# Performance work log

Measured on AMD Instinct MI355X. Metric: run time of the kernel, lower is better.

The kernel has to match this reference:

```python
import jax, jax.numpy as jnp
import numpy as np

B, IN, H = 4096, 1024, 1024

def setup_inputs() -> dict:
    key = jax.random.key(0)
    ks = jax.random.split(key, 8)
    s = 1.0 / np.sqrt(IN + H)  # ~torch Linear init scale
    return {
        "x": jax.random.normal(ks[0], (B, IN), jnp.float32),
        "h_prev": jax.random.normal(ks[1], (B, H), jnp.float32),
        "c_prev": jax.random.normal(ks[2], (B, H), jnp.float32),
        "Wf": jax.random.normal(ks[3], (IN + H, H), jnp.float32) * s,
        "bf": jnp.zeros((H,), jnp.float32),
        "Wi": jax.random.normal(ks[4], (IN + H, H), jnp.float32) * s,
        "bi": jnp.zeros((H,), jnp.float32),
        "Wg": jax.random.normal(ks[5], (IN + H, H), jnp.float32) * s,
        "bg": jnp.zeros((H,), jnp.float32),
        "Wo": jax.random.normal(ks[6], (IN + H, H), jnp.float32) * s,
        "bo": jnp.zeros((H,), jnp.float32),
    }

def reference(x, h_prev, c_prev, Wf, bf, Wi, bi, Wg, bg, Wo, bo):
    combined = jnp.concatenate([x, h_prev], axis=1)          # [B, IN+H]
    # fuse the 4 gate projections into one GEMM: [B, IN+H] x [IN+H, 4H]
    W = jnp.concatenate([Wf, Wi, Wg, Wo], axis=1)            # [IN+H, 4H]
    b = jnp.concatenate([bf, bi, bg, bo], axis=0)            # [4H]
    gates = combined @ W + b                                  # [B, 4H]
    f_t, i_t, g_t, o_t = jnp.split(gates, 4, axis=1)
    f_t = jax.nn.sigmoid(f_t)
    i_t = jax.nn.sigmoid(i_t)
    g_t = jnp.tanh(g_t)
    o_t = jax.nn.sigmoid(o_t)
    c_next = f_t * c_prev + i_t * g_t
    h_next = o_t * jnp.tanh(c_next)
    return (h_next, c_next)
```

## Files before the change

kernel.cpp:

```cpp
#include <hip/hip_runtime.h>

#define B_DIM 4096
#define H_DIM 1024
#define K_DIM 2048
#define NTILE (K_DIM / 64)

typedef unsigned short u16;
typedef unsigned int u32;
typedef __attribute__((ext_vector_type(8))) short short8;
typedef __attribute__((ext_vector_type(4))) float f32x4;

typedef const __attribute__((address_space(1))) void* gas_ptr;
typedef __attribute__((address_space(3))) void* las_ptr;

#define WT_ELEMS (4 * H_DIM * K_DIM)
#define AC_ELEMS (B_DIM * K_DIM)
#define WS_NEEDED ((size_t)(WT_ELEMS + AC_ELEMS) * 2)

__device__ __forceinline__ void gl_lds16(const u16* g, u16* l) {
    __builtin_amdgcn_global_load_lds((gas_ptr)g, (las_ptr)l, 16, 0, 0);
}
__device__ __forceinline__ float bf2f(u16 v) {
    return __builtin_bit_cast(float, (u32)((u32)v << 16));
}
__device__ __forceinline__ u16 f2bf(float f) {
    u32 u = __builtin_bit_cast(u32, f);
    return (u16)((u + 0x7fffu + ((u >> 16) & 1u)) >> 16);
}
__device__ __forceinline__ float sigm(float x) { return 1.0f / (1.0f + __expf(-x)); }
__device__ __forceinline__ float tanh_f(float x) { return 1.0f - 2.0f / (__expf(2.0f * x) + 1.0f); }

__global__ __launch_bounds__(256) void prep_all(const float* __restrict__ x, const float* __restrict__ h,
                                                const float* __restrict__ Wf, const float* __restrict__ Wi,
                                                const float* __restrict__ Wg, const float* __restrict__ Wo,
                                                u16* __restrict__ A, u16* __restrict__ Wt) {
    const int t = threadIdx.x;
    if (blockIdx.x < 4096) {
        int e = (blockIdx.x * 256 + t) * 8;
        int m = e >> 11, c = e & 2047;
        const float* src = (c < 1024) ? (x + (size_t)m * 1024 + c) : (h + (size_t)m * 1024 + (c - 1024));
        float4 v0 = ((const float4*)src)[0], v1 = ((const float4*)src)[1];
        short8 q;
        q[0] = (short)f2bf(v0.x); q[1] = (short)f2bf(v0.y); q[2] = (short)f2bf(v0.z); q[3] = (short)f2bf(v0.w);
        q[4] = (short)f2bf(v1.x); q[5] = (short)f2bf(v1.y); q[6] = (short)f2bf(v1.z); q[7] = (short)f2bf(v1.w);
        *(short8*)(A + e) = q;
    } else {
        const int id = (blockIdx.x - 4096) * 4 + (t >> 6);
        const int l = t & 63;
        const int k0 = (id & 31) * 64, n0 = ((id >> 5) & 15) * 64, g = id >> 9;
        const float* W = (g == 0) ? Wf : (g == 1) ? Wi : (g == 2) ? Wg : Wo;
        const int no = (l & 7) * 8;
        const int ko = (l >> 3) * 8;
        float f[8][8];
#pragma unroll
        for (int j = 0; j < 8; ++j) {
            const float4* s = (const float4*)(W + (size_t)(k0 + ko + j) * H_DIM + n0 + no);
            float4 a = s[0], b = s[1];
            f[j][0] = a.x; f[j][1] = a.y; f[j][2] = a.z; f[j][3] = a.w;
            f[j][4] = b.x; f[j][5] = b.y; f[j][6] = b.z; f[j][7] = b.w;
        }
        u16* dst0 = Wt + (size_t)g * ((size_t)H_DIM * K_DIM) + (size_t)(n0 + no) * K_DIM + k0 + ko;
#pragma unroll
        for (int w2 = 0; w2 < 8; ++w2) {
            short8 q;
#pragma unroll
            for (int j = 0; j < 8; ++j) q[j] = (short)f2bf(f[j][w2]);
            *(short8*)(dst0 + (size_t)w2 * K_DIM) = q;
        }
    }
}

#define PH_OPEN                                                  \
    __builtin_amdgcn_s_barrier();                                \
    asm volatile("s_waitcnt lgkmcnt(0)" ::: "memory");           \
    __builtin_amdgcn_sched_barrier(0);                           \
    __builtin_amdgcn_s_setprio(1)

#define PH_CLOSE                                                 \
    __builtin_amdgcn_s_setprio(0);                               \
    __builtin_amdgcn_sched_barrier(0);                           \
    __builtin_amdgcn_s_barrier();                                \
    __builtin_amdgcn_sched_barrier(0)

#define PH_CLOSE_VM2                                             \
    __builtin_amdgcn_s_setprio(0);                               \
    __builtin_amdgcn_sched_barrier(0);                           \
    asm volatile("s_waitcnt vmcnt(2)" ::: "memory");             \
    __builtin_amdgcn_s_barrier();                                \
    __builtin_amdgcn_sched_barrier(0)

#define PH_CLOSE_VM0                                             \
    __builtin_amdgcn_s_setprio(0);                               \
    __builtin_amdgcn_sched_barrier(0);                           \
    asm volatile("s_waitcnt vmcnt(0)" ::: "memory");             \
    __builtin_amdgcn_s_barrier();                                \
    __builtin_amdgcn_sched_barrier(0)

#define STG_A(NB, H)                                                              \
    gl_lds16(pa[H][0], &sm[NB][(H) * 8192 + t * 8]);        pa[H][0] += 64;       \
    gl_lds16(pa[H][1], &sm[NB][(H) * 8192 + 4096 + t * 8]); pa[H][1] += 64;

#define STG_B(NB, H)                                                                      \
    gl_lds16(pb[H][0], &sm[NB][16384 + (H) * 8192 + t * 8]);        pb[H][0] += 64;       \
    gl_lds16(pb[H][1], &sm[NB][16384 + (H) * 8192 + 4096 + t * 8]); pb[H][1] += 64;

#define RD_A(CB, KS)                                                                       \
    _Pragma("unroll") for (int mi = 0; mi < 8; ++mi)                                       \
        afr[mi] = *(const short8*)&sm[CB][(wr * 128 + mi * 16 + l15) * 64 +                \
                                          ((((KS) * 4 + quad) ^ v7) * 8)];

#define RD_B(CB, G, KS)                                                                    \
    (*(const short8*)&sm[CB][16384 + (G) * 4096 + (wc * 16 + l15) * 64 +                   \
                             ((((KS) * 4 + quad) ^ v7) * 8)])

#define MFMA_PAIR(GP)                                                                      \
    _Pragma("unroll") for (int mi = 0; mi < 8; ++mi)                                       \
        acc[mi][2 * (GP)] = __builtin_amdgcn_mfma_f32_16x16x32_bf16(                       \
            afr[mi], b0, acc[mi][2 * (GP)], 0, 0, 0);                                      \
    _Pragma("unroll") for (int mi = 0; mi < 8; ++mi)                                       \
        acc[mi][2 * (GP) + 1] = __builtin_amdgcn_mfma_f32_16x16x32_bf16(                   \
            afr[mi], b1, acc[mi][2 * (GP) + 1], 0, 0, 0);

__global__ __launch_bounds__(512, 2) void lstm_gemm(
    const u16* __restrict__ A, const u16* __restrict__ Wt, const float* __restrict__ c_prev,
    const float* __restrict__ bf_, const float* __restrict__ bi_,
    const float* __restrict__ bg_, const float* __restrict__ bo_,
    float* __restrict__ out) {
    __shared__ u16 sm[2][32768];

    const int t = threadIdx.x;
    const int w = t >> 6;
    const int l = t & 63;
    const int quad = l >> 4;
    const int l15 = l & 15;
    const int v7 = l15 & 7;
    const int wr = w >> 2;
    const int wc = w & 3;
    const int m0 = blockIdx.x * 256;
    const int j0 = blockIdx.y * 64;

    f32x4 acc[8][4];
#pragma unroll
    for (int mi = 0; mi < 8; ++mi)
#pragma unroll
        for (int g = 0; g < 4; ++g)
            acc[mi][g] = (f32x4){0.f, 0.f, 0.f, 0.f};

    const u16* pa[2][2];
    const u16* pb[2][2];
#pragma unroll
    for (int h = 0; h < 2; ++h)
#pragma unroll
        for (int i = 0; i < 2; ++i) {
            int e = h * 8192 + (i * 512 + t) * 8;
            int m = e >> 6, sl = (e >> 3) & 7;
            pa[h][i] = A + (size_t)(m0 + m) * K_DIM + ((sl ^ (m & 7)) * 8);
            int g = e >> 12, n = (e >> 6) & 63;
            pb[h][i] = Wt + (size_t)g * ((size_t)H_DIM * K_DIM) + (size_t)(j0 + n) * K_DIM +
                       ((sl ^ (n & 7)) * 8);
        }

    short8 afr[8], b0, b1;

    STG_A(0, 0); STG_A(0, 1); STG_B(0, 0); STG_B(0, 1);
    asm volatile("s_waitcnt vmcnt(2)" ::: "memory");
    __builtin_amdgcn_s_barrier();
    __builtin_amdgcn_sched_barrier(0);

    for (int kt = 0; kt < NTILE - 1; ++kt) {
        const int cb = kt & 1, nb = cb ^ 1;
        RD_A(cb, 0);
        b0 = RD_B(cb, 0, 0); b1 = RD_B(cb, 1, 0);
        STG_A(nb, 0);
        PH_OPEN;
        MFMA_PAIR(0);
        PH_CLOSE_VM2;
        b0 = RD_B(cb, 2, 0); b1 = RD_B(cb, 3, 0);
        STG_A(nb, 1);
        PH_OPEN;
        MFMA_PAIR(1);
        PH_CLOSE;
        RD_A(cb, 1);
        b0 = RD_B(cb, 0, 1); b1 = RD_B(cb, 1, 1);
        STG_B(nb, 0);
        PH_OPEN;
        MFMA_PAIR(0);
        PH_CLOSE;
        b0 = RD_B(cb, 2, 1); b1 = RD_B(cb, 3, 1);
        STG_B(nb, 1);
        PH_OPEN;
        MFMA_PAIR(1);
        PH_CLOSE_VM2;
    }
    {
        const int cb = (NTILE - 1) & 1;
        RD_A(cb, 0);
        b0 = RD_B(cb, 0, 0); b1 = RD_B(cb, 1, 0);
        PH_OPEN;
        MFMA_PAIR(0);
        PH_CLOSE_VM0;
        b0 = RD_B(cb, 2, 0); b1 = RD_B(cb, 3, 0);
        PH_OPEN;
        MFMA_PAIR(1);
        PH_CLOSE;
        RD_A(cb, 1);
        b0 = RD_B(cb, 0, 1); b1 = RD_B(cb, 1, 1);
        PH_OPEN;
        MFMA_PAIR(0);
        PH_CLOSE;
        b0 = RD_B(cb, 2, 1); b1 = RD_B(cb, 3, 1);
        asm volatile("s_waitcnt lgkmcnt(0)" ::: "memory");
        __builtin_amdgcn_sched_barrier(0);
        MFMA_PAIR(1);
    }

    const int col = j0 + wc * 16 + l15;
    const float bF = bf_[col], bI = bi_[col], bG = bg_[col], bO = bo_[col];
#pragma unroll
    for (int mi = 0; mi < 8; ++mi) {
        const int rowbase = m0 + wr * 128 + mi * 16 + quad * 4;
        float cp[4];
#pragma unroll
        for (int rr = 0; rr < 4; ++rr)
            cp[rr] = c_prev[(size_t)(rowbase + rr) * H_DIM + col];
#pragma unroll
        for (int rr = 0; rr < 4; ++rr) {
            float fv = sigm(acc[mi][0][rr] + bF);
            float iv = sigm(acc[mi][1][rr] + bI);
            float gv = tanh_f(acc[mi][2][rr] + bG);
            float ov = sigm(acc[mi][3][rr] + bO);
            float cn = fv * cp[rr] + iv * gv;
            float hn = ov * tanh_f(cn);
            size_t idx = (size_t)(rowbase + rr) * H_DIM + col;
            out[idx] = hn;
            out[(size_t)B_DIM * H_DIM + idx] = cn;
        }
    }
}

__global__ __launch_bounds__(256) void lstm_f32(
    const float* __restrict__ x, const float* __restrict__ h_prev, const float* __restrict__ c_prev,
    const float* __restrict__ Wf, const float* __restrict__ Wi, const float* __restrict__ Wg, const float* __restrict__ Wo,
    const float* __restrict__ bf_, const float* __restrict__ bi_, const float* __restrict__ bg_, const float* __restrict__ bo_,
    float* __restrict__ out) {
    __shared__ u16 smem[16384];
    u16* sA = smem;
    u16* sB = smem + 4096;

    const int t = threadIdx.x;
    const int w = t >> 6;
    const int l = t & 63;
    const int quad = l >> 4;
    const int l15 = l & 15;
    const int wr = w >> 1;
    const int wc = w & 1;
    const int m0 = blockIdx.x * 128;
    const int j0 = blockIdx.y * 32;

    const int arow = t >> 1;
    const int akh = (t & 1) * 16;
    const int r7 = t & 127;
    const int bk = r7 >> 2;
    const int bn8 = (r7 & 3) * 8;
    const int kswz = ((((bk >> 3) ^ (bn8 >> 3)) << 3) | (bk & 7));
    const float* WpA = (t < 128) ? Wf : Wi;
    const float* WpB = (t < 128) ? Wg : Wo;
    const int gA = (t >> 7);
    const int gB = 2 + (t >> 7);

    f32x4 acc[2][4][2];
#pragma unroll
    for (int gi = 0; gi < 2; ++gi)
#pragma unroll
        for (int mi = 0; mi < 4; ++mi)
#pragma unroll
            for (int ni = 0; ni < 2; ++ni)
                acc[gi][mi][ni] = (f32x4){0.f, 0.f, 0.f, 0.f};

    for (int kt = 0; kt < K_DIM / 32; ++kt) {
        const float* srcA = (kt < 32) ? x : h_prev;
        const int koff = (kt & 31) * 32;
        __syncthreads();

        const float4* ap = (const float4*)(srcA + (size_t)(m0 + arow) * H_DIM + koff + akh);
        float4 a0 = ap[0], a1 = ap[1], a2 = ap[2], a3 = ap[3];
        short8 p0, p1;
        p0[0] = (short)f2bf(a0.x); p0[1] = (short)f2bf(a0.y); p0[2] = (short)f2bf(a0.z); p0[3] = (short)f2bf(a0.w);
        p0[4] = (short)f2bf(a1.x); p0[5] = (short)f2bf(a1.y); p0[6] = (short)f2bf(a1.z); p0[7] = (short)f2bf(a1.w);
        p1[0] = (short)f2bf(a2.x); p1[1] = (short)f2bf(a2.y); p1[2] = (short)f2bf(a2.z); p1[3] = (short)f2bf(a2.w);
        p1[4] = (short)f2bf(a3.x); p1[5] = (short)f2bf(a3.y); p1[6] = (short)f2bf(a3.z); p1[7] = (short)f2bf(a3.w);
        *(short8*)(sA + arow * 32 + akh) = p0;
        *(short8*)(sA + arow * 32 + akh + 8) = p1;

        const float* gpA = WpA + (size_t)(kt * 32 + bk) * H_DIM + j0 + bn8;
        const float* gpB = WpB + (size_t)(kt * 32 + bk) * H_DIM + j0 + bn8;
        float4 c0 = *(const float4*)gpA, c1 = *(const float4*)(gpA + 4);
        float4 d0 = *(const float4*)gpB, d1 = *(const float4*)(gpB + 4);
        sB[gA * 1024 + (bn8 + 0) * 32 + kswz] = f2bf(c0.x);
        sB[gA * 1024 + (bn8 + 1) * 32 + kswz] = f2bf(c0.y);
        sB[gA * 1024 + (bn8 + 2) * 32 + kswz] = f2bf(c0.z);
        sB[gA * 1024 + (bn8 + 3) * 32 + kswz] = f2bf(c0.w);
        sB[gA * 1024 + (bn8 + 4) * 32 + kswz] = f2bf(c1.x);
        sB[gA * 1024 + (bn8 + 5) * 32 + kswz] = f2bf(c1.y);
        sB[gA * 1024 + (bn8 + 6) * 32 + kswz] = f2bf(c1.z);
        sB[gA * 1024 + (bn8 + 7) * 32 + kswz] = f2bf(c1.w);
        sB[gB * 1024 + (bn8 + 0) * 32 + kswz] = f2bf(d0.x);
        sB[gB * 1024 + (bn8 + 1) * 32 + kswz] = f2bf(d0.y);
        sB[gB * 1024 + (bn8 + 2) * 32 + kswz] = f2bf(d0.z);
        sB[gB * 1024 + (bn8 + 3) * 32 + kswz] = f2bf(d0.w);
        sB[gB * 1024 + (bn8 + 4) * 32 + kswz] = f2bf(d1.x);
        sB[gB * 1024 + (bn8 + 5) * 32 + kswz] = f2bf(d1.y);
        sB[gB * 1024 + (bn8 + 6) * 32 + kswz] = f2bf(d1.z);
        sB[gB * 1024 + (bn8 + 7) * 32 + kswz] = f2bf(d1.w);
        __syncthreads();

        short8 bfr[2][2];
#pragma unroll
        for (int gi = 0; gi < 2; ++gi) {
            int g = wc * 2 + gi;
#pragma unroll
            for (int ni = 0; ni < 2; ++ni) {
                int n = ni * 16 + l15;
                bfr[gi][ni] = *(const short8*)(sB + g * 1024 + n * 32 + ((quad ^ (n >> 3)) * 8));
            }
        }
#pragma unroll
        for (int mi = 0; mi < 4; ++mi) {
            int m = wr * 64 + mi * 16 + l15;
            short8 afr = *(const short8*)(sA + m * 32 + quad * 8);
#pragma unroll
            for (int gi = 0; gi < 2; ++gi)
#pragma unroll
                for (int ni = 0; ni < 2; ++ni)
                    acc[gi][mi][ni] =
                        __builtin_amdgcn_mfma_f32_16x16x32_bf16(afr, bfr[gi][ni], acc[gi][mi][ni], 0, 0, 0);
        }
    }

    __syncthreads();
#pragma unroll
    for (int gi = 0; gi < 2; ++gi) {
        int g = wc * 2 + gi;
        const float* bp = (g == 0) ? bf_ : (g == 1) ? bi_ : (g == 2) ? bg_ : bo_;
#pragma unroll
        for (int ni = 0; ni < 2; ++ni) {
            int col = ni * 16 + l15;
            float bias = bp[j0 + col];
#pragma unroll
            for (int mi = 0; mi < 4; ++mi)
#pragma unroll
                for (int rr = 0; rr < 4; ++rr) {
                    int row = wr * 64 + mi * 16 + quad * 4 + rr;
                    float v = acc[gi][mi][ni][rr] + bias;
                    v = (g == 2) ? tanh_f(v) : sigm(v);
                    smem[g * 4096 + row * 32 + col] = f2bf(v);
                }
        }
    }
    __syncthreads();

    const int col = t & 31;
    const int rb = t >> 5;
#pragma unroll
    for (int p = 0; p < 16; ++p) {
        int row = p * 8 + rb;
        float fv = bf2f(smem[0 * 4096 + row * 32 + col]);
        float iv = bf2f(smem[1 * 4096 + row * 32 + col]);
        float gv = bf2f(smem[2 * 4096 + row * 32 + col]);
        float ov = bf2f(smem[3 * 4096 + row * 32 + col]);
        size_t oidx = (size_t)(m0 + row) * H_DIM + j0 + col;
        float cp = c_prev[oidx];
        float cn = fv * cp + iv * gv;
        float hn = ov * tanh_f(cn);
        out[oidx] = hn;
        out[(size_t)B_DIM * H_DIM + oidx] = cn;
    }
}

extern "C" void kernel_launch(void* const* d_in, const int* in_sizes, int n_in,
                              void* d_out, int out_size, void* d_ws, size_t ws_size,
                              hipStream_t stream) {
    const float* x   = (const float*)d_in[0];
    const float* hp  = (const float*)d_in[1];
    const float* cp  = (const float*)d_in[2];
    const float* Wf  = (const float*)d_in[3];
    const float* bf_ = (const float*)d_in[4];
    const float* Wi  = (const float*)d_in[5];
    const float* bi_ = (const float*)d_in[6];
    const float* Wg  = (const float*)d_in[7];
    const float* bg_ = (const float*)d_in[8];
    const float* Wo  = (const float*)d_in[9];
    const float* bo_ = (const float*)d_in[10];

    if (ws_size >= WS_NEEDED) {
        u16* Wt = (u16*)d_ws;
        u16* Ac = (u16*)d_ws + WT_ELEMS;
        prep_all<<<dim3(4096 + 512), dim3(256), 0, stream>>>(x, hp, Wf, Wi, Wg, Wo, Ac, Wt);
        lstm_gemm<<<dim3(B_DIM / 256, H_DIM / 64), dim3(512), 0, stream>>>(
            Ac, Wt, cp, bf_, bi_, bg_, bo_, (float*)d_out);
    } else {
        lstm_f32<<<dim3(B_DIM / 128, H_DIM / 32), dim3(256), 0, stream>>>(
            x, hp, cp, Wf, Wi, Wg, Wo, bf_, bi_, bg_, bo_, (float*)d_out);
    }
}
```

Measured before the change: 209.4 us.

## Fuse activation bf16 conversion into GEMM A-tile staging

Removes the separate pre-pass that converted and concatenated x and h_prev into a bf16 workspace. The GEMM now reads fp32 x/h directly into registers, converts to bf16 and writes the swizzled LDS tile itself, with the loads spread across the pipeline phases and the wait counts adjusted. This saves a 16 MB read, an 8 MB write and the 8 MB reread of the converted activations. In exchange, each of the 16 column blocks reconverts the same A rows, the GEMM reads twice the bytes per A tile, and the loop gains register pressure and VALU work for the conversions.

After: 246.9 us. 17.9% more time.

```diff
diff --git a/kernel.cpp b/kernel.cpp
--- a/kernel.cpp
+++ b/kernel.cpp
@@ -8,14 +8,14 @@
 typedef unsigned short u16;
 typedef unsigned int u32;
 typedef __attribute__((ext_vector_type(8))) short short8;
+typedef __attribute__((ext_vector_type(4))) short s16x4;
 typedef __attribute__((ext_vector_type(4))) float f32x4;
 
 typedef const __attribute__((address_space(1))) void* gas_ptr;
 typedef __attribute__((address_space(3))) void* las_ptr;
 
 #define WT_ELEMS (4 * H_DIM * K_DIM)
-#define AC_ELEMS (B_DIM * K_DIM)
-#define WS_NEEDED ((size_t)(WT_ELEMS + AC_ELEMS) * 2)
+#define WS_NEEDED ((size_t)WT_ELEMS * 2)
 
 __device__ __forceinline__ void gl_lds16(const u16* g, u16* l) {
     __builtin_amdgcn_global_load_lds((gas_ptr)g, (las_ptr)l, 16, 0, 0);
@@ -27,46 +27,39 @@
     u32 u = __builtin_bit_cast(u32, f);
     return (u16)((u + 0x7fffu + ((u >> 16) & 1u)) >> 16);
 }
+__device__ __forceinline__ s16x4 cvt4(float4 v) {
+    s16x4 r;
+    r[0] = (short)f2bf(v.x); r[1] = (short)f2bf(v.y);
+    r[2] = (short)f2bf(v.z); r[3] = (short)f2bf(v.w);
+    return r;
+}
 __device__ __forceinline__ float sigm(float x) { return 1.0f / (1.0f + __expf(-x)); }
 __device__ __forceinline__ float tanh_f(float x) { return 1.0f - 2.0f / (__expf(2.0f * x) + 1.0f); }
 
-__global__ __launch_bounds__(256) void prep_all(const float* __restrict__ x, const float* __restrict__ h,
-                                                const float* __restrict__ Wf, const float* __restrict__ Wi,
-                                                const float* __restrict__ Wg, const float* __restrict__ Wo,
-                                                u16* __restrict__ A, u16* __restrict__ Wt) {
-    const int t = threadIdx.x;
-    if (blockIdx.x < 4096) {
-        int e = (blockIdx.x * 256 + t) * 8;
-        int m = e >> 11, c = e & 2047;
-        const float* src = (c < 1024) ? (x + (size_t)m * 1024 + c) : (h + (size_t)m * 1024 + (c - 1024));
-        float4 v0 = ((const float4*)src)[0], v1 = ((const float4*)src)[1];
+__global__ __launch_bounds__(256) void prep_W(const float* __restrict__ Wf, const float* __restrict__ Wi,
+                                              const float* __restrict__ Wg, const float* __restrict__ Wo,
+                                              u16* __restrict__ Wt) {
+    const int id = blockIdx.x * 4 + ((int)threadIdx.x >> 6);
+    const int l = threadIdx.x & 63;
+    const int k0 = (id & 31) * 64, n0 = ((id >> 5) & 15) * 64, g = id >> 9;
+    const float* W = (g == 0) ? Wf : (g == 1) ? Wi : (g == 2) ? Wg : Wo;
+    const int no = (l & 7) * 8;
+    const int ko = (l >> 3) * 8;
+    float f[8][8];
+#pragma unroll
+    for (int j = 0; j < 8; ++j) {
+        const float4* s = (const float4*)(W + (size_t)(k0 + ko + j) * H_DIM + n0 + no);
+        float4 a = s[0], b = s[1];
+        f[j][0] = a.x; f[j][1] = a.y; f[j][2] = a.z; f[j][3] = a.w;
+        f[j][4] = b.x; f[j][5] = b.y; f[j][6] = b.z; f[j][7] = b.w;
+    }
+    u16* dst0 = Wt + (size_t)g * ((size_t)H_DIM * K_DIM) + (size_t)(n0 + no) * K_DIM + k0 + ko;
+#pragma unroll
+    for (int w2 = 0; w2 < 8; ++w2) {
         short8 q;
-        q[0] = (short)f2bf(v0.x); q[1] = (short)f2bf(v0.y); q[2] = (short)f2bf(v0.z); q[3] = (short)f2bf(v0.w);
-        q[4] = (short)f2bf(v1.x); q[5] = (short)f2bf(v1.y); q[6] = (short)f2bf(v1.z); q[7] = (short)f2bf(v1.w);
-        *(short8*)(A + e) = q;
-    } else {
-        const int id = (blockIdx.x - 4096) * 4 + (t >> 6);
-        const int l = t & 63;
-        const int k0 = (id & 31) * 64, n0 = ((id >> 5) & 15) * 64, g = id >> 9;
-        const float* W = (g == 0) ? Wf : (g == 1) ? Wi : (g == 2) ? Wg : Wo;
-        const int no = (l & 7) * 8;
-        const int ko = (l >> 3) * 8;
-        float f[8][8];
-#pragma unroll
-        for (int j = 0; j < 8; ++j) {
-            const float4* s = (const float4*)(W + (size_t)(k0 + ko + j) * H_DIM + n0 + no);
-            float4 a = s[0], b = s[1];
-            f[j][0] = a.x; f[j][1] = a.y; f[j][2] = a.z; f[j][3] = a.w;
-            f[j][4] = b.x; f[j][5] = b.y; f[j][6] = b.z; f[j][7] = b.w;
-        }
-        u16* dst0 = Wt + (size_t)g * ((size_t)H_DIM * K_DIM) + (size_t)(n0 + no) * K_DIM + k0 + ko;
-#pragma unroll
-        for (int w2 = 0; w2 < 8; ++w2) {
-            short8 q;
-#pragma unroll
-            for (int j = 0; j < 8; ++j) q[j] = (short)f2bf(f[j][w2]);
-            *(short8*)(dst0 + (size_t)w2 * K_DIM) = q;
-        }
+#pragma unroll
+        for (int j = 0; j < 8; ++j) q[j] = (short)f2bf(f[j][w2]);
+        *(short8*)(dst0 + (size_t)w2 * K_DIM) = q;
     }
 }
 
@@ -82,10 +75,17 @@
     __builtin_amdgcn_s_barrier();                                \
     __builtin_amdgcn_sched_barrier(0)
 
-#define PH_CLOSE_VM2                                             \
+#define PH_CLOSE_VM4                                             \
     __builtin_amdgcn_s_setprio(0);                               \
     __builtin_amdgcn_sched_barrier(0);                           \
-    asm volatile("s_waitcnt vmcnt(2)" ::: "memory");             \
+    asm volatile("s_waitcnt vmcnt(4)" ::: "memory");             \
+    __builtin_amdgcn_s_barrier();                                \
+    __builtin_amdgcn_sched_barrier(0)
+
+#define PH_CLOSE_VM2_LG0                                         \
+    __builtin_amdgcn_s_setprio(0);                               \
+    __builtin_amdgcn_sched_barrier(0);                           \
+    asm volatile("s_waitcnt vmcnt(2) lgkmcnt(0)" ::: "memory");  \
     __builtin_amdgcn_s_barrier();                                \
     __builtin_amdgcn_sched_barrier(0)
 
@@ -96,13 +96,13 @@
     __builtin_amdgcn_s_barrier();                                \
     __builtin_amdgcn_sched_barrier(0)
 
-#define STG_A(NB, H)                                                              \
-    gl_lds16(pa[H][0], &sm[NB][(H) * 8192 + t * 8]);        pa[H][0] += 64;       \
-    gl_lds16(pa[H][1], &sm[NB][(H) * 8192 + 4096 + t * 8]); pa[H][1] += 64;
-
 #define STG_B(NB, H)                                                                      \
     gl_lds16(pb[H][0], &sm[NB][16384 + (H) * 8192 + t * 8]);        pb[H][0] += 64;       \
     gl_lds16(pb[H][1], &sm[NB][16384 + (H) * 8192 + 4096 + t * 8]); pb[H][1] += 64;
+
+#define WR_A(NB, J0)                                                                      \
+    _Pragma("unroll") for (int j = (J0); j < (J0) + 4; ++j)                               \
+        *(s16x4*)&sm[NB][(arow + j * 32) * 64 + aswz] = cvt4(afv[j]);
 
 #define RD_A(CB, KS)                                                                       \
     _Pragma("unroll") for (int mi = 0; mi < 8; ++mi)                                       \
@@ -122,7 +122,8 @@
             afr[mi], b1, acc[mi][2 * (GP) + 1], 0, 0, 0);
 
 __global__ __launch_bounds__(512, 2) void lstm_gemm(
-    const u16* __restrict__ A, const u16* __restrict__ Wt, const float* __restrict__ c_prev,
+    const float* __restrict__ xg, const float* __restrict__ hg,
+    const u16* __restrict__ Wt, const float* __restrict__ c_prev,
     const float* __restrict__ bf_, const float* __restrict__ bi_,
     const float* __restrict__ bg_, const float* __restrict__ bo_,
     float* __restrict__ out) {
@@ -139,6 +140,10 @@
     const int m0 = blockIdx.x * 256;
     const int j0 = blockIdx.y * 64;
 
+    const int arow = t >> 4;
+    const int acol = (t & 15) * 4;
+    const int aswz = (((t & 15) >> 1) ^ ((t >> 4) & 7)) * 8 + (t & 1) * 4;
+
     f32x4 acc[8][4];
 #pragma unroll
     for (int mi = 0; mi < 8; ++mi)
@@ -146,51 +151,62 @@
         for (int g = 0; g < 4; ++g)
             acc[mi][g] = (f32x4){0.f, 0.f, 0.f, 0.f};
 
-    const u16* pa[2][2];
     const u16* pb[2][2];
 #pragma unroll
     for (int h = 0; h < 2; ++h)
 #pragma unroll
         for (int i = 0; i < 2; ++i) {
             int e = h * 8192 + (i * 512 + t) * 8;
-            int m = e >> 6, sl = (e >> 3) & 7;
-            pa[h][i] = A + (size_t)(m0 + m) * K_DIM + ((sl ^ (m & 7)) * 8);
+            int sl = (e >> 3) & 7;
             int g = e >> 12, n = (e >> 6) & 63;
             pb[h][i] = Wt + (size_t)g * ((size_t)H_DIM * K_DIM) + (size_t)(j0 + n) * K_DIM +
                        ((sl ^ (n & 7)) * 8);
         }
 
     short8 afr[8], b0, b1;
-
-    STG_A(0, 0); STG_A(0, 1); STG_B(0, 0); STG_B(0, 1);
-    asm volatile("s_waitcnt vmcnt(2)" ::: "memory");
-    __builtin_amdgcn_s_barrier();
-    __builtin_amdgcn_sched_barrier(0);
+    float4 afv[8];
+
+    {
+        const float4* ab0 = (const float4*)(xg + (size_t)(m0 + arow) * 1024 + acol);
+#pragma unroll
+        for (int j = 0; j < 8; ++j) afv[j] = ab0[j * 8192];
+        STG_B(0, 0); STG_B(0, 1);
+        WR_A(0, 0); WR_A(0, 4);
+        asm volatile("s_waitcnt vmcnt(2) lgkmcnt(0)" ::: "memory");
+        __builtin_amdgcn_s_barrier();
+        __builtin_amdgcn_sched_barrier(0);
+    }
 
     for (int kt = 0; kt < NTILE - 1; ++kt) {
         const int cb = kt & 1, nb = cb ^ 1;
+        const int T = kt + 1;
+        const float* srcA = (T < 16) ? xg : hg;
+        const float4* abase =
+            (const float4*)(srcA + (size_t)(m0 + arow) * 1024 + (T & 15) * 64 + acol);
         RD_A(cb, 0);
         b0 = RD_B(cb, 0, 0); b1 = RD_B(cb, 1, 0);
-        STG_A(nb, 0);
+        afv[0] = abase[0]; afv[1] = abase[8192]; afv[2] = abase[16384]; afv[3] = abase[24576];
         PH_OPEN;
         MFMA_PAIR(0);
-        PH_CLOSE_VM2;
+        PH_CLOSE_VM4;
         b0 = RD_B(cb, 2, 0); b1 = RD_B(cb, 3, 0);
-        STG_A(nb, 1);
+        afv[4] = abase[32768]; afv[5] = abase[40960]; afv[6] = abase[49152]; afv[7] = abase[57344];
         PH_OPEN;
         MFMA_PAIR(1);
         PH_CLOSE;
         RD_A(cb, 1);
         b0 = RD_B(cb, 0, 1); b1 = RD_B(cb, 1, 1);
+        WR_A(nb, 0);
         STG_B(nb, 0);
         PH_OPEN;
         MFMA_PAIR(0);
         PH_CLOSE;
         b0 = RD_B(cb, 2, 1); b1 = RD_B(cb, 3, 1);
+        WR_A(nb, 4);
         STG_B(nb, 1);
         PH_OPEN;
         MFMA_PAIR(1);
-        PH_CLOSE_VM2;
+        PH_CLOSE_VM2_LG0;
     }
     {
         const int cb = (NTILE - 1) & 1;
@@ -394,10 +410,9 @@
 
     if (ws_size >= WS_NEEDED) {
         u16* Wt = (u16*)d_ws;
-        u16* Ac = (u16*)d_ws + WT_ELEMS;
-        prep_all<<<dim3(4096 + 512), dim3(256), 0, stream>>>(x, hp, Wf, Wi, Wg, Wo, Ac, Wt);
+        prep_W<<<dim3(512), dim3(256), 0, stream>>>(Wf, Wi, Wg, Wo, Wt);
         lstm_gemm<<<dim3(B_DIM / 256, H_DIM / 64), dim3(512), 0, stream>>>(
-            Ac, Wt, cp, bf_, bi_, bg_, bo_, (float*)d_out);
+            x, hp, Wt, cp, bf_, bi_, bg_, bo_, (float*)d_out);
     } else {
         lstm_f32<<<dim3(B_DIM / 128, H_DIM / 32), dim3(256), 0, stream>>>(
             x, hp, cp, Wf, Wi, Wg, Wo, bf_, bi_, bg_, bo_, (float*)d_out);
```
